# Kernel tuning notes

Measured on AMD Instinct MI355X. Metric: run time of the kernel, lower is better.

Reference implementation:

```python
import jax, jax.numpy as jnp
import numpy as np

EXTENT = 3.0            # 'radius' arg of the model is passed as extents to ContinuousConv
SEARCH_R = EXTENT / 2.0 # Open3D fixed_radius_search uses extents/2
KS = 6                  # kernel_size [6,6,6]
N, K = 10000, 32
EPS = 1e-12
FOUR_OVER_PI = float(4.0 / np.pi)


def ball_to_cube_volume_preserving(u):
    # u: [...,3] in the unit ball -> cube [-1,1]^3 (Open3D mapping:
    # MapSphereToCylinder followed by MapCylinderToCube).
    x, y, z = u[..., 0], u[..., 1], u[..., 2]
    sq = x * x + y * y + z * z
    norm = jnp.sqrt(jnp.maximum(sq, EPS))
    rho2 = x * x + y * y
    # sphere -> cylinder (volume preserving, two regions)
    in_cone = 1.25 * z * z > rho2
    s1 = jnp.sqrt(3.0 * norm / (norm + jnp.abs(z)))
    s2 = norm / jnp.sqrt(jnp.maximum(rho2, EPS))
    s = jnp.where(in_cone, s1, s2)
    xc = x * s
    yc = y * s
    zc = jnp.where(in_cone, jnp.sign(z) * norm, 1.5 * z)
    tiny = sq < EPS
    xc = jnp.where(tiny, 0.0, xc)
    yc = jnp.where(tiny, 0.0, yc)
    zc = jnp.where(tiny, 0.0, zc)
    # cylinder -> cube (inverse concentric / Shirley-Chiu map on xy disc)
    sq_xy = xc * xc + yc * yc
    norm_xy = jnp.sqrt(jnp.maximum(sq_xy, EPS))
    x_major = jnp.abs(yc) <= jnp.abs(xc)
    xd = jnp.where(jnp.abs(xc) < EPS, 1.0, xc)
    yd = jnp.where(jnp.abs(yc) < EPS, 1.0, yc)
    tx = jnp.sign(xc) * norm_xy
    ty = jnp.sign(yc) * norm_xy
    xq = jnp.where(x_major, tx, ty * FOUR_OVER_PI * jnp.arctan(xc / yd))
    yq = jnp.where(x_major, tx * FOUR_OVER_PI * jnp.arctan(yc / xd), ty)
    tiny_xy = sq_xy < EPS
    xq = jnp.where(tiny_xy, 0.0, xq)
    yq = jnp.where(tiny_xy, 0.0, yq)
    return jnp.stack([xq, yq, zc], axis=-1)


def continuous_conv(feats, pos, nidx, nmask, W, b):
    # feats [N,Cin], pos [N,3], nidx [N,K] int32 (padded), nmask [N,K] bool
    # W [KS,KS,KS,Cin,Cout], b [Cout]
    n, k = nidx.shape
    Cin, Cout = W.shape[3], W.shape[4]
    M = KS * KS * KS
    maskf = nmask.astype(feats.dtype)
    u = (pos[nidx] - pos[:, None, :]) * (2.0 / EXTENT)          # [N,K,3], unit ball
    coords = (ball_to_cube_volume_preserving(u) + 1.0) * (0.5 * (KS - 1))  # align_corners
    i0f = jnp.floor(coords)
    frac = coords - i0f
    i0 = jnp.clip(i0f.astype(jnp.int32), 0, KS - 1)
    i1 = jnp.minimum(i0 + 1, KS - 1)
    fN = feats[nidx]                                            # [N,K,Cin]
    base = jnp.arange(n, dtype=jnp.int32)[:, None] * M          # [N,1]
    # Scatter trilinear-weighted neighbor features into per-point kernel cells:
    # A[j, cell, :] = sum_{neighbors k, corners c} w_{j,k,c} * feats[nidx[j,k]]
    A = jnp.zeros((n * M, Cin), feats.dtype)
    for cx in (0, 1):
        ix = i1[..., 0] if cx else i0[..., 0]
        wx = frac[..., 0] if cx else 1.0 - frac[..., 0]
        for cy in (0, 1):
            iy = i1[..., 1] if cy else i0[..., 1]
            wy = frac[..., 1] if cy else 1.0 - frac[..., 1]
            for cz in (0, 1):
                iz = i1[..., 2] if cz else i0[..., 2]
                wz = frac[..., 2] if cz else 1.0 - frac[..., 2]
                w = wx * wy * wz * maskf                        # [N,K]
                flat = (base + (ix * KS + iy) * KS + iz).reshape(-1)
                A = A.at[flat].add((w[..., None] * fN).reshape(n * k, Cin))
    out = jnp.einsum('nmc,mco->no', A.reshape(n, M, Cin), W.reshape(M, Cin, Cout))
    # normalize=True (Open3D default): divide by neighbor count, guarded for empty
    cnt = maskf.sum(axis=1, keepdims=True)
    out = jnp.where(cnt > 0, out / jnp.maximum(cnt, 1.0), out)
    return jax.nn.relu(out + b)                                 # use_bias + activation


def setup_inputs() -> dict:
    rng = np.random.default_rng(0)
    L = 16.0  # box side -> ~32 neighbors on average within SEARCH_R
    pos = (rng.random((N, 3)) * L).astype(np.float32)
    nidx = np.zeros((N, K), np.int32)
    nmask = np.zeros((N, K), bool)
    chunk = 512
    for s in range(0, N, chunk):
        d2 = ((pos[s:s + chunk, None, :] - pos[None, :, :]) ** 2).sum(-1)
        part = np.argpartition(d2, K, axis=1)[:, :K].astype(np.int32)
        m = np.take_along_axis(d2, part, axis=1) <= SEARCH_R * SEARCH_R
        nidx[s:s + chunk] = np.where(m, part, 0)
        nmask[s:s + chunk] = m

    def p(*shape):
        return jnp.asarray((rng.standard_normal(shape) * 0.1).astype(np.float32))

    return {
        'feats': jnp.asarray(rng.standard_normal((N, 4)).astype(np.float32)),
        'pos': jnp.asarray(pos),
        'neighbor_idx': jnp.asarray(nidx),
        'neighbor_mask': jnp.asarray(nmask),
        'W1': p(KS, KS, KS, 4, 64), 'b1': jnp.zeros((64,), jnp.float32),
        'W2': p(KS, KS, KS, 64, 64), 'b2': jnp.zeros((64,), jnp.float32),
        'W3': p(KS, KS, KS, 64, 32), 'b3': jnp.zeros((32,), jnp.float32),
        'Wfc1': p(32, 64), 'bfc1': jnp.zeros((64,), jnp.float32),
        'Wfc2': p(64, 64), 'bfc2': jnp.zeros((64,), jnp.float32),
        'Wfc3': p(64, 32), 'bfc3': jnp.zeros((32,), jnp.float32),
        'Wout': p(32, 3), 'bout': jnp.zeros((3,), jnp.float32),
    }


def reference(feats, pos, neighbor_idx, neighbor_mask, W1, b1, W2, b2, W3, b3,
              Wfc1, bfc1, Wfc2, bfc2, Wfc3, bfc3, Wout, bout):
    x = continuous_conv(feats, pos, neighbor_idx, neighbor_mask, W1, b1)
    x = continuous_conv(x, pos, neighbor_idx, neighbor_mask, W2, b2)
    x = continuous_conv(x, pos, neighbor_idx, neighbor_mask, W3, b3)
    x = jax.nn.relu(x @ Wfc1 + bfc1)
    x = jax.nn.relu(x @ Wfc2 + bfc2)
    x = jax.nn.relu(x @ Wfc3 + bfc3)
    return x @ Wout + bout
```

## Files before the change

### kernel.cpp

```cpp
#include <hip/hip_runtime.h>
#include <math.h>

#define NPTS  10000
#define KNB   32
#define NCELL 216
#define NSGT  157

__device__ __forceinline__ float sgnf(float v) {
    return (v > 0.0f) ? 1.0f : ((v < 0.0f) ? -1.0f : 0.0f);
}

__device__ __forceinline__ void ball_to_cube(float x, float y, float z,
                                             float& X, float& Y, float& Z) {
    const float EPSF = 1e-12f;
    const float FOPI = (float)(4.0 / 3.14159265358979323846);
    float sq   = x * x + y * y + z * z;
    float norm = sqrtf(fmaxf(sq, EPSF));
    float rho2 = x * x + y * y;
    bool in_cone = (1.25f * z * z > rho2);
    float s1 = sqrtf(3.0f * norm / (norm + fabsf(z)));
    float s2 = norm / sqrtf(fmaxf(rho2, EPSF));
    float s  = in_cone ? s1 : s2;
    float xc = x * s;
    float yc = y * s;
    float zc = in_cone ? sgnf(z) * norm : 1.5f * z;
    if (sq < EPSF) { xc = 0.0f; yc = 0.0f; zc = 0.0f; }
    float sq_xy   = xc * xc + yc * yc;
    float norm_xy = sqrtf(fmaxf(sq_xy, EPSF));
    bool x_major = (fabsf(yc) <= fabsf(xc));
    float xd = (fabsf(xc) < EPSF) ? 1.0f : xc;
    float yd = (fabsf(yc) < EPSF) ? 1.0f : yc;
    float tx = sgnf(xc) * norm_xy;
    float ty = sgnf(yc) * norm_xy;
    float xq = x_major ? tx : ty * FOPI * atanf(xc / yd);
    float yq = x_major ? tx * FOPI * atanf(yc / xd) : ty;
    if (sq_xy < EPSF) { xq = 0.0f; yq = 0.0f; }
    X = xq; Y = yq; Z = zc;
}

__global__ __launch_bounds__(256) void geom_kernel(
    const float* __restrict__ pos, const int* __restrict__ nidx,
    uint4* __restrict__ geo, float* __restrict__ cnt) {
    int t = blockIdx.x * 256 + threadIdx.x;
    if (t >= NPTS * KNB) return;
    int j = t >> 5;
    int k = t & 31;
    int nid = nidx[t];
    float px = pos[j * 3], py = pos[j * 3 + 1], pz = pos[j * 3 + 2];
    float qx = pos[nid * 3], qy = pos[nid * 3 + 1], qz = pos[nid * 3 + 2];
    float dx = __fsub_rn(px, qx), dy = __fsub_rn(py, qy), dz = __fsub_rn(pz, qz);
    float d2 = __fadd_rn(__fadd_rn(__fmul_rn(dx, dx), __fmul_rn(dy, dy)),
                         __fmul_rn(dz, dz));
    bool valid = (d2 <= 2.25f);
    if (valid && nid == 0) {
        for (int kk = 0; kk < k; ++kk) {
            if (nidx[j * KNB + kk] == 0) { valid = false; break; }
        }
    }
    uint4 g = make_uint4(0u, 0u, 0u, 0u);
    if (valid) {
        const float C = (float)(2.0 / 3.0);
        float ux = (qx - px) * C, uy = (qy - py) * C, uz = (qz - pz) * C;
        float X, Y, Z;
        ball_to_cube(ux, uy, uz, X, Y, Z);
        float cs[3] = { (X + 1.0f) * 2.5f, (Y + 1.0f) * 2.5f, (Z + 1.0f) * 2.5f };
        int i0[3], i1[3];
        float fr[3];
        #pragma unroll
        for (int d = 0; d < 3; ++d) {
            float f0 = floorf(cs[d]);
            fr[d] = cs[d] - f0;
            int a = (int)f0;
            a = min(max(a, 0), 5);
            i0[d] = a;
            i1[d] = min(a + 1, 5);
        }
        int c000 = (i0[0] * 6 + i0[1]) * 6 + i0[2];
        unsigned bits = (unsigned)c000
                      | ((unsigned)(i1[0] - i0[0]) << 8)
                      | ((unsigned)(i1[1] - i0[1]) << 9)
                      | ((unsigned)(i1[2] - i0[2]) << 10)
                      | (1u << 11)
                      | ((unsigned)nid << 12);
        g.x = __float_as_uint(fr[0]);
        g.y = __float_as_uint(fr[1]);
        g.z = __float_as_uint(fr[2]);
        g.w = bits;
        atomicAdd(&cnt[j], 1.0f);
    }
    geo[t] = g;
}

__global__ __launch_bounds__(256) void sort_kernel(
    const uint4* __restrict__ geo, uint2* __restrict__ contribs,
    int* __restrict__ starts) {
    __shared__ int hist[NCELL];
    __shared__ int pref[NCELL + 1];
    const int sg = blockIdx.x, tid = threadIdx.x;
    if (tid < NCELL) hist[tid] = 0;
    __syncthreads();
    const int npts = min(64, NPTS - sg * 64);
    const int nrec = npts * KNB;
    const uint4* gb = geo + (size_t)sg * 64 * KNB;
    for (int r = tid; r < nrec; r += 256) {
        uint4 g = gb[r];
        if (g.w & 2048u) {
            int c000 = g.w & 255u;
            int dxo = (g.w & 256u)  ? 36 : 0;
            int dyo = (g.w & 512u)  ? 6  : 0;
            int dzo = (g.w & 1024u) ? 1  : 0;
            #pragma unroll
            for (int c = 0; c < 8; ++c) {
                int cell = c000 + ((c & 4) ? dxo : 0) + ((c & 2) ? dyo : 0)
                                + ((c & 1) ? dzo : 0);
                atomicAdd(&hist[cell], 1);
            }
        }
    }
    __syncthreads();
    if (tid == 0) {
        int run = 0;
        for (int m = 0; m < NCELL; ++m) { pref[m] = run; run += hist[m]; }
        pref[NCELL] = run;
    }
    __syncthreads();
    for (int i = tid; i < NCELL + 1; i += 256)
        starts[sg * (NCELL + 1) + i] = pref[i];
    if (tid < NCELL) hist[tid] = pref[tid];
    __syncthreads();
    uint2* cb = contribs + (size_t)sg * 16384;
    for (int r = tid; r < nrec; r += 256) {
        uint4 g = gb[r];
        if (g.w & 2048u) {
            int ptl = r >> 5;
            float fx = __uint_as_float(g.x);
            float fy = __uint_as_float(g.y);
            float fz = __uint_as_float(g.z);
            int c000 = g.w & 255u;
            int dxo = (g.w & 256u)  ? 36 : 0;
            int dyo = (g.w & 512u)  ? 6  : 0;
            int dzo = (g.w & 1024u) ? 1  : 0;
            int nid = (g.w >> 12) & 16383u;
            #pragma unroll
            for (int c = 0; c < 8; ++c) {
                float wgt = ((c & 4) ? fx : 1.f - fx)
                          * ((c & 2) ? fy : 1.f - fy)
                          * ((c & 1) ? fz : 1.f - fz);
                int cell = c000 + ((c & 4) ? dxo : 0) + ((c & 2) ? dyo : 0)
                                + ((c & 1) ? dzo : 0);
                int p = atomicAdd(&hist[cell], 1);
                cb[p] = make_uint2(__float_as_uint(wgt),
                                   (unsigned)nid | ((unsigned)ptl << 14)
                                                 | ((unsigned)cell << 20));
            }
        }
    }
}

template<int CIN, int COUT, int CPC, int KSPLIT>
__global__ __launch_bounds__(COUT * 8, 6) void conv_kernel(
    const float* __restrict__ feats, const float* __restrict__ W,
    const uint2* __restrict__ contribs, const int* __restrict__ starts,
    float* __restrict__ partial) {
    constexpr int KC   = CPC * CIN;
    constexpr int ASTR = KC + 4;
    constexpr int BT   = COUT * 8;
    constexpr int NCHUNK = NCELL / CPC;
    constexpr int TPC  = CIN / 4;
    constexpr int GPB  = BT / TPC;

    __shared__ alignas(16) float Ab[2][64 * ASTR];

    const int tid   = threadIdx.x;
    const int lane  = tid & 63;
    const int wvid  = __builtin_amdgcn_readfirstlane(tid >> 6);
    const int cow   = wvid * 8;
    const int bx    = blockIdx.x;
    const int ks    = blockIdx.y;
    const int gslot = tid / TPC;
    const int ch    = tid % TPC;

    const uint2* cbs = contribs + (size_t)bx * 16384;
    const int*   st  = starts + bx * (NCELL + 1);

    const int c0 = NCHUNK * ks / KSPLIT;
    const int c1 = NCHUNK * (ks + 1) / KSPLIT;

    auto zero = [&](int b) {
        float4 z; z.x = z.y = z.z = z.w = 0.f;
        float4* p = reinterpret_cast<float4*>(Ab[b]);
        #pragma unroll 2
        for (int i = tid; i < 64 * ASTR / 4; i += BT) p[i] = z;
    };
    auto scatter = [&](int c, int b) {
        const int s = st[c * CPC], e = st[c * CPC + CPC];
        const int cb4 = c * CPC;
        for (int i = s + gslot; i < e; i += GPB) {
            uint2 rec = cbs[i];
            float wgt = __uint_as_float(rec.x);
            int nid = rec.y & 16383;
            int ptl = (rec.y >> 14) & 63;
            int cel = (int)(rec.y >> 20);
            float4 f4 = *reinterpret_cast<const float4*>(
                feats + (size_t)nid * CIN + ch * 4);
            float* dst = &Ab[b][ptl * ASTR + (cel - cb4) * CIN + ch * 4];
            atomicAdd(dst + 0, wgt * f4.x);
            atomicAdd(dst + 1, wgt * f4.y);
            atomicAdd(dst + 2, wgt * f4.z);
            atomicAdd(dst + 3, wgt * f4.w);
        }
    };

    zero(0); zero(1);
    __syncthreads();
    scatter(c0, 0);
    __syncthreads();

    float acc[8];
    #pragma unroll
    for (int j = 0; j < 8; ++j) acc[j] = 0.f;

    for (int c = c0; c < c1; ++c) {
        const int b = (c - c0) & 1;
        if (c + 1 < c1) scatter(c + 1, b ^ 1);
        const float* Wc = W + (size_t)c * CPC * CIN * COUT;
        const float* Ar = Ab[b] + lane * ASTR;
        #pragma unroll 4
        for (int g = 0; g < KC / 4; ++g) {
            float4 a4 = *reinterpret_cast<const float4*>(Ar + g * 4);
            const float av[4] = { a4.x, a4.y, a4.z, a4.w };
            #pragma unroll
            for (int j = 0; j < 4; ++j) {
                float4 w0 = *reinterpret_cast<const float4*>(
                    Wc + (size_t)(g * 4 + j) * COUT + cow);
                float4 w1 = *reinterpret_cast<const float4*>(
                    Wc + (size_t)(g * 4 + j) * COUT + cow + 4);
                float a = av[j];
                acc[0] = fmaf(a, w0.x, acc[0]);
                acc[1] = fmaf(a, w0.y, acc[1]);
                acc[2] = fmaf(a, w0.z, acc[2]);
                acc[3] = fmaf(a, w0.w, acc[3]);
                acc[4] = fmaf(a, w1.x, acc[4]);
                acc[5] = fmaf(a, w1.y, acc[5]);
                acc[6] = fmaf(a, w1.z, acc[6]);
                acc[7] = fmaf(a, w1.w, acc[7]);
            }
        }
        __syncthreads();
        zero(b);
        __syncthreads();
    }

    const int n = bx * 64 + lane;
    if (n < NPTS) {
        float* po = partial + ((size_t)ks * NPTS + n) * COUT + cow;
        *reinterpret_cast<float4*>(po)     = make_float4(acc[0], acc[1], acc[2], acc[3]);
        *reinterpret_cast<float4*>(po + 4) = make_float4(acc[4], acc[5], acc[6], acc[7]);
    }
}

template<int COUT, int KSPLIT>
__global__ __launch_bounds__(256) void combine_kernel(
    const float* __restrict__ partial, const float* __restrict__ cnt,
    const float* __restrict__ bias, float* __restrict__ out) {
    int idx = blockIdx.x * 256 + threadIdx.x;
    if (idx >= NPTS * COUT) return;
    int n = idx / COUT, co = idx % COUT;
    float s = 0.f;
    #pragma unroll
    for (int k2 = 0; k2 < KSPLIT; ++k2)
        s += partial[((size_t)k2 * NPTS + n) * COUT + co];
    float c = cnt[n];
    if (c > 0.f) s /= fmaxf(c, 1.f);
    out[idx] = fmaxf(s + bias[co], 0.f);
}

__global__ __launch_bounds__(64) void fc_kernel(
    const float* __restrict__ x,
    const float* __restrict__ W1, const float* __restrict__ b1,
    const float* __restrict__ W2, const float* __restrict__ b2,
    const float* __restrict__ W3, const float* __restrict__ b3,
    const float* __restrict__ W4, const float* __restrict__ b4,
    float* __restrict__ out) {
    int n = blockIdx.x;
    int lane = threadIdx.x;
    float xv = (lane < 32) ? x[(size_t)n * 32 + lane] : 0.0f;

    float t = b1[lane];
    for (int ci = 0; ci < 32; ++ci)
        t = fmaf(__shfl(xv, ci), W1[ci * 64 + lane], t);
    float h1 = fmaxf(t, 0.0f);

    t = b2[lane];
    for (int ci = 0; ci < 64; ++ci)
        t = fmaf(__shfl(h1, ci), W2[ci * 64 + lane], t);
    float h2 = fmaxf(t, 0.0f);

    int l32 = lane & 31;
    t = b3[l32];
    for (int ci = 0; ci < 64; ++ci)
        t = fmaf(__shfl(h2, ci), W3[ci * 32 + l32], t);
    float h3 = fmaxf(t, 0.0f);

    int ch = (lane < 3) ? lane : 0;
    float o = b4[ch];
    for (int ci = 0; ci < 32; ++ci)
        o = fmaf(__shfl(h3, ci), W4[ci * 3 + ch], o);
    if (lane < 3) out[(size_t)n * 3 + lane] = o;
}

extern "C" void kernel_launch(void* const* d_in, const int* in_sizes, int n_in,
                              void* d_out, int out_size, void* d_ws, size_t ws_size,
                              hipStream_t stream) {
    const float* feats = (const float*)d_in[0];
    const float* pos   = (const float*)d_in[1];
    const int*   nidx  = (const int*)d_in[2];
    const float* W1 = (const float*)d_in[4];
    const float* b1 = (const float*)d_in[5];
    const float* W2 = (const float*)d_in[6];
    const float* b2 = (const float*)d_in[7];
    const float* W3 = (const float*)d_in[8];
    const float* b3 = (const float*)d_in[9];
    const float* Wfc1 = (const float*)d_in[10];
    const float* bfc1 = (const float*)d_in[11];
    const float* Wfc2 = (const float*)d_in[12];
    const float* bfc2 = (const float*)d_in[13];
    const float* Wfc3 = (const float*)d_in[14];
    const float* bfc3 = (const float*)d_in[15];
    const float* Wout = (const float*)d_in[16];
    const float* bout = (const float*)d_in[17];

    char* ws = (char*)d_ws;
    uint2* contrib = (uint2*)(ws);
    int*   starts  = (int*)  (ws + 20578304);
    float* cnt     = (float*)(ws + 20714624);
    float* x1      = (float*)(ws + 20754624);
    float* x2      = (float*)(ws + 23314624);
    float* x3      = (float*)(ws + 25874624);
    uint4* geo     = (uint4*)(ws + 27154624);
    float* partial = (float*)(ws + 27154624);

    const bool big = ws_size >= (size_t)47634624;

    hipMemsetAsync(cnt, 0, NPTS * sizeof(float), stream);
    geom_kernel<<<(NPTS * KNB) / 256, 256, 0, stream>>>(pos, nidx, geo, cnt);
    sort_kernel<<<NSGT, 256, 0, stream>>>(geo, contrib, starts);

    conv_kernel<4, 64, 8, 4><<<dim3(NSGT, 4), 512, 0, stream>>>(
        feats, W1, contrib, starts, partial);
    combine_kernel<64, 4><<<(NPTS * 64 + 255) / 256, 256, 0, stream>>>(
        partial, cnt, b1, x1);

    if (big) {
        conv_kernel<64, 64, 1, 8><<<dim3(NSGT, 8), 512, 0, stream>>>(
            x1, W2, contrib, starts, partial);
        combine_kernel<64, 8><<<(NPTS * 64 + 255) / 256, 256, 0, stream>>>(
            partial, cnt, b2, x2);
    } else {
        conv_kernel<64, 64, 1, 4><<<dim3(NSGT, 4), 512, 0, stream>>>(
            x1, W2, contrib, starts, partial);
        combine_kernel<64, 4><<<(NPTS * 64 + 255) / 256, 256, 0, stream>>>(
            partial, cnt, b2, x2);
    }

    conv_kernel<64, 32, 1, 8><<<dim3(NSGT, 8), 256, 0, stream>>>(
        x2, W3, contrib, starts, partial);
    combine_kernel<32, 8><<<(NPTS * 32 + 255) / 256, 256, 0, stream>>>(
        partial, cnt, b3, x3);

    fc_kernel<<<NPTS, 64, 0, stream>>>(x3, Wfc1, bfc1, Wfc2, bfc2,
                                       Wfc3, bfc3, Wout, bout, (float*)d_out);
}
```

Before: 2.078 ms.

## Register-tile conv GEMM over 128 points per block with unrolled scatter

Each conv block now handles two 64-point segments (128 points) with 256 threads. Each thread computes a 4-point by 8-or-4-channel register tile, so every weight load is reused across four points instead of one. The per-segment start offsets are staged in shared memory, and the scatter loop is unrolled by four so record and feature loads are issued ahead of the LDS atomics. The costs are double the LDS footprint, more registers (launch bounds now allow only 2 blocks), and half as many blocks, which may reduce occupancy and latency hiding.

```diff
diff --git a/kernel.cpp b/kernel.cpp
--- a/kernel.cpp
+++ b/kernel.cpp
@@ -158,30 +158,37 @@
 }
 
 template<int CIN, int COUT, int CPC, int KSPLIT>
-__global__ __launch_bounds__(COUT * 8, 6) void conv_kernel(
+__global__ __launch_bounds__(256, 2) void conv_kernel(
     const float* __restrict__ feats, const float* __restrict__ W,
     const uint2* __restrict__ contribs, const int* __restrict__ starts,
     float* __restrict__ partial) {
     constexpr int KC   = CPC * CIN;
     constexpr int ASTR = KC + 4;
-    constexpr int BT   = COUT * 8;
     constexpr int NCHUNK = NCELL / CPC;
+    constexpr int Q4   = COUT / 32;
     constexpr int TPC  = CIN / 4;
-    constexpr int GPB  = BT / TPC;
-
-    __shared__ alignas(16) float Ab[2][64 * ASTR];
-
-    const int tid   = threadIdx.x;
-    const int lane  = tid & 63;
-    const int wvid  = __builtin_amdgcn_readfirstlane(tid >> 6);
-    const int cow   = wvid * 8;
-    const int bx    = blockIdx.x;
-    const int ks    = blockIdx.y;
-    const int gslot = tid / TPC;
+    constexpr int SLOT = 128 / TPC;
+    constexpr int U    = 4;
+
+    __shared__ alignas(16) float Ab[2][128 * ASTR];
+    __shared__ int Sl[2][NCELL + 1];
+
+    const int tid = threadIdx.x;
+    const int ptg = tid >> 3;
+    const int cog = tid & 7;
+    const int bx  = blockIdx.x;
+    const int ks  = blockIdx.y;
+
+    const int sgl   = tid >> 7;
+    const int lslot = (tid & 127) / TPC;
     const int ch    = tid % TPC;
-
-    const uint2* cbs = contribs + (size_t)bx * 16384;
-    const int*   st  = starts + bx * (NCELL + 1);
+    const uint2* cbs = contribs + (size_t)(bx * 2 + sgl) * 16384;
+
+    for (int s2 = 0; s2 < 2; ++s2) {
+        int sg = bx * 2 + s2;
+        for (int i = tid; i < NCELL + 1; i += 256)
+            Sl[s2][i] = (sg < NSGT) ? starts[sg * (NCELL + 1) + i] : 0;
+    }
 
     const int c0 = NCHUNK * ks / KSPLIT;
     const int c1 = NCHUNK * (ks + 1) / KSPLIT;
@@ -189,25 +196,42 @@
     auto zero = [&](int b) {
         float4 z; z.x = z.y = z.z = z.w = 0.f;
         float4* p = reinterpret_cast<float4*>(Ab[b]);
-        #pragma unroll 2
-        for (int i = tid; i < 64 * ASTR / 4; i += BT) p[i] = z;
+        for (int i = tid; i < 128 * ASTR / 4; i += 256) p[i] = z;
     };
     auto scatter = [&](int c, int b) {
-        const int s = st[c * CPC], e = st[c * CPC + CPC];
-        const int cb4 = c * CPC;
-        for (int i = s + gslot; i < e; i += GPB) {
-            uint2 rec = cbs[i];
-            float wgt = __uint_as_float(rec.x);
-            int nid = rec.y & 16383;
-            int ptl = (rec.y >> 14) & 63;
-            int cel = (int)(rec.y >> 20);
-            float4 f4 = *reinterpret_cast<const float4*>(
-                feats + (size_t)nid * CIN + ch * 4);
-            float* dst = &Ab[b][ptl * ASTR + (cel - cb4) * CIN + ch * 4];
-            atomicAdd(dst + 0, wgt * f4.x);
-            atomicAdd(dst + 1, wgt * f4.y);
-            atomicAdd(dst + 2, wgt * f4.z);
-            atomicAdd(dst + 3, wgt * f4.w);
+        const int cb = c * CPC;
+        const int s = Sl[sgl][cb], e = Sl[sgl][cb + CPC];
+        float* Abase = Ab[b] + sgl * 64 * ASTR;
+        int i = s + lslot;
+        while (i < e) {
+            uint2 recs[U];
+            #pragma unroll
+            for (int u = 0; u < U; ++u) {
+                int idx = i + u * SLOT;
+                recs[u] = cbs[min(idx, e - 1)];
+            }
+            float4 f4[U];
+            #pragma unroll
+            for (int u = 0; u < U; ++u) {
+                int nid = recs[u].y & 16383;
+                f4[u] = *reinterpret_cast<const float4*>(
+                    feats + (size_t)nid * CIN + ch * 4);
+            }
+            #pragma unroll
+            for (int u = 0; u < U; ++u) {
+                int idx = i + u * SLOT;
+                if (idx < e) {
+                    float wgt = __uint_as_float(recs[u].x);
+                    int ptl = (recs[u].y >> 14) & 63;
+                    int cel = (int)(recs[u].y >> 20);
+                    float* dst = Abase + ptl * ASTR + (cel - cb) * CIN + ch * 4;
+                    atomicAdd(dst + 0, wgt * f4[u].x);
+                    atomicAdd(dst + 1, wgt * f4[u].y);
+                    atomicAdd(dst + 2, wgt * f4[u].z);
+                    atomicAdd(dst + 3, wgt * f4[u].w);
+                }
+            }
+            i += U * SLOT;
         }
     };
 
@@ -216,34 +240,45 @@
     scatter(c0, 0);
     __syncthreads();
 
-    float acc[8];
+    float4 acc[4][Q4];
     #pragma unroll
-    for (int j = 0; j < 8; ++j) acc[j] = 0.f;
+    for (int p = 0; p < 4; ++p)
+        #pragma unroll
+        for (int q = 0; q < Q4; ++q) { acc[p][q].x = acc[p][q].y = acc[p][q].z = acc[p][q].w = 0.f; }
 
     for (int c = c0; c < c1; ++c) {
         const int b = (c - c0) & 1;
         if (c + 1 < c1) scatter(c + 1, b ^ 1);
-        const float* Wc = W + (size_t)c * CPC * CIN * COUT;
-        const float* Ar = Ab[b] + lane * ASTR;
-        #pragma unroll 4
+        const float* Wc = W + (size_t)c * KC * COUT + cog * (Q4 * 4);
+        const float* Ablk = Ab[b] + ptg * 4 * ASTR;
+        #pragma unroll 2
         for (int g = 0; g < KC / 4; ++g) {
-            float4 a4 = *reinterpret_cast<const float4*>(Ar + g * 4);
-            const float av[4] = { a4.x, a4.y, a4.z, a4.w };
+            float4 wv[4][Q4];
             #pragma unroll
             for (int j = 0; j < 4; ++j) {
-                float4 w0 = *reinterpret_cast<const float4*>(
-                    Wc + (size_t)(g * 4 + j) * COUT + cow);
-                float4 w1 = *reinterpret_cast<const float4*>(
-                    Wc + (size_t)(g * 4 + j) * COUT + cow + 4);
-                float a = av[j];
-                acc[0] = fmaf(a, w0.x, acc[0]);
-                acc[1] = fmaf(a, w0.y, acc[1]);
-                acc[2] = fmaf(a, w0.z, acc[2]);
-                acc[3] = fmaf(a, w0.w, acc[3]);
-                acc[4] = fmaf(a, w1.x, acc[4]);
-                acc[5] = fmaf(a, w1.y, acc[5]);
-                acc[6] = fmaf(a, w1.z, acc[6]);
-                acc[7] = fmaf(a, w1.w, acc[7]);
+                const float* wp = Wc + (size_t)(g * 4 + j) * COUT;
+                #pragma unroll
+                for (int q = 0; q < Q4; ++q)
+                    wv[j][q] = *reinterpret_cast<const float4*>(wp + q * 4);
+            }
+            float4 av[4];
+            #pragma unroll
+            for (int p = 0; p < 4; ++p)
+                av[p] = *reinterpret_cast<const float4*>(Ablk + p * ASTR + g * 4);
+            #pragma unroll
+            for (int p = 0; p < 4; ++p) {
+                const float* ap = reinterpret_cast<const float*>(&av[p]);
+                #pragma unroll
+                for (int j = 0; j < 4; ++j) {
+                    float a = ap[j];
+                    #pragma unroll
+                    for (int q = 0; q < Q4; ++q) {
+                        acc[p][q].x = fmaf(a, wv[j][q].x, acc[p][q].x);
+                        acc[p][q].y = fmaf(a, wv[j][q].y, acc[p][q].y);
+                        acc[p][q].z = fmaf(a, wv[j][q].z, acc[p][q].z);
+                        acc[p][q].w = fmaf(a, wv[j][q].w, acc[p][q].w);
+                    }
+                }
             }
         }
         __syncthreads();
@@ -251,11 +286,15 @@
         __syncthreads();
     }
 
-    const int n = bx * 64 + lane;
-    if (n < NPTS) {
-        float* po = partial + ((size_t)ks * NPTS + n) * COUT + cow;
-        *reinterpret_cast<float4*>(po)     = make_float4(acc[0], acc[1], acc[2], acc[3]);
-        *reinterpret_cast<float4*>(po + 4) = make_float4(acc[4], acc[5], acc[6], acc[7]);
+    #pragma unroll
+    for (int p = 0; p < 4; ++p) {
+        int n = bx * 128 + ptg * 4 + p;
+        if (n < NPTS) {
+            float* po = partial + ((size_t)ks * NPTS + n) * COUT + cog * (Q4 * 4);
+            #pragma unroll
+            for (int q = 0; q < Q4; ++q)
+                *reinterpret_cast<float4*>(po + q * 4) = acc[p][q];
+        }
     }
 }
 
@@ -346,24 +385,24 @@
     geom_kernel<<<(NPTS * KNB) / 256, 256, 0, stream>>>(pos, nidx, geo, cnt);
     sort_kernel<<<NSGT, 256, 0, stream>>>(geo, contrib, starts);
 
-    conv_kernel<4, 64, 8, 4><<<dim3(NSGT, 4), 512, 0, stream>>>(
+    conv_kernel<4, 64, 8, 4><<<dim3(79, 4), 256, 0, stream>>>(
         feats, W1, contrib, starts, partial);
     combine_kernel<64, 4><<<(NPTS * 64 + 255) / 256, 256, 0, stream>>>(
         partial, cnt, b1, x1);
 
     if (big) {
-        conv_kernel<64, 64, 1, 8><<<dim3(NSGT, 8), 512, 0, stream>>>(
+        conv_kernel<64, 64, 1, 8><<<dim3(79, 8), 256, 0, stream>>>(
             x1, W2, contrib, starts, partial);
         combine_kernel<64, 8><<<(NPTS * 64 + 255) / 256, 256, 0, stream>>>(
             partial, cnt, b2, x2);
     } else {
-        conv_kernel<64, 64, 1, 4><<<dim3(NSGT, 4), 512, 0, stream>>>(
+        conv_kernel<64, 64, 1, 4><<<dim3(79, 4), 256, 0, stream>>>(
             x1, W2, contrib, starts, partial);
         combine_kernel<64, 4><<<(NPTS * 64 + 255) / 256, 256, 0, stream>>>(
             partial, cnt, b2, x2);
     }
 
-    conv_kernel<64, 32, 1, 8><<<dim3(NSGT, 8), 256, 0, stream>>>(
+    conv_kernel<64, 32, 1, 8><<<dim3(79, 8), 256, 0, stream>>>(
         x2, W3, contrib, starts, partial);
     combine_kernel<32, 8><<<(NPTS * 32 + 255) / 256, 256, 0, stream>>>(
         partial, cnt, b3, x3);
```

Result: slower. 2.497 ms (+20.2%).
